# Optimization experiments

Hardware: AMD Instinct MI355X
Metric: run time of the kernel (lower is better)

## Reference

```python
import jax, jax.numpy as jnp
import numpy as np
from jax import lax

ITERATIONS = 8
KT, KH, KW = 3, 7, 7


def _ssm_op(left, right):
    a1, b1 = left
    a2, b2 = right
    return (a1 * a2, a2 * b1 + b2)


def setup_inputs() -> dict:
    key = jax.random.key(0)
    k1, k2, k3 = jax.random.split(key, 3)
    B, T, H, W, C = 1, 16, 64, 64, 128
    x = jax.random.normal(k1, (B, T, H, W, C), dtype=jnp.float32)
    A_kernel = 0.02 * jax.random.normal(k2, (C, KT, KH, KW), dtype=jnp.float32)
    B_kernel = 0.02 * jax.random.normal(k3, (C, KT, KH, KW), dtype=jnp.float32)
    return {"x": x, "A_kernel": A_kernel, "B_kernel": B_kernel}


def _pad_kernel_fft(kern, T, H, W):
    # Place (C, kt, kh, kw) kernel circularly centered into a (C, T, H, W) canvas, FFT it.
    C = kern.shape[0]
    t_idx = (jnp.arange(KT) - KT // 2) % T
    h_idx = (jnp.arange(KH) - KH // 2) % H
    w_idx = (jnp.arange(KW) - KW // 2) % W
    tt, th, tw = jnp.meshgrid(t_idx, h_idx, w_idx, indexing="ij")
    padded = jnp.zeros((C, T, H, W), dtype=kern.dtype).at[:, tt, th, tw].set(kern)
    kf = jnp.fft.fftn(padded, axes=(1, 2, 3))  # (C, T, H, W) complex
    return kf.transpose(1, 2, 3, 0)[None, ...]  # (1, T, H, W, C)


def reference(x, A_kernel, B_kernel):
    B, T, H, W, C = x.shape
    A_stable = 0.9 * jnp.tanh(A_kernel)
    A_f = _pad_kernel_fft(A_stable, T, H, W)   # (1,T,H,W,C)
    B_f = _pad_kernel_fft(B_kernel, T, H, W)   # (1,T,H,W,C)
    x_f = jnp.fft.fftn(x, axes=(1, 2, 3))      # (B,T,H,W,C)
    Bx_f = B_f * x_f
    a_seq = jnp.broadcast_to(A_f, (ITERATIONS, B, T, H, W, C))
    b_seq = jnp.broadcast_to(Bx_f, (ITERATIONS, B, T, H, W, C))
    _, h_all_f = lax.associative_scan(_ssm_op, (a_seq, b_seq), axis=0)
    h_final = jnp.fft.ifftn(h_all_f[-1], axes=(1, 2, 3)).real
    return h_final
```

## Files before the change

### kernel.cpp

```cpp
#include <hip/hip_runtime.h>
#include <hip/hip_fp16.h>
#include <math.h>

#define TT 16
#define HH 64
#define WW 64
#define CC 128

#define LROW(r) (((r) & 0x38) | ((((r) >> 3) ^ (r)) & 7))

__device__ __forceinline__ float2 cadd(float2 a, float2 b){ return make_float2(a.x+b.x, a.y+b.y); }
__device__ __forceinline__ float2 csub(float2 a, float2 b){ return make_float2(a.x-b.x, a.y-b.y); }
__device__ __forceinline__ float2 cmul(float2 a, float2 b) {
    return make_float2(a.x*b.x - a.y*b.y, a.x*b.y + a.y*b.x);
}
__device__ __forceinline__ float2 cmac(float2 acc, float2 a, float2 b) {
    acc.x = fmaf(a.x, b.x, fmaf(-a.y, b.y, acc.x));
    acc.y = fmaf(a.x, b.y, fmaf(a.y, b.x, acc.y));
    return acc;
}
__device__ __forceinline__ float2 csq(float2 a) {
    return make_float2(a.x*a.x - a.y*a.y, 2.f*a.x*a.y);
}

template<int SGN>
__device__ __forceinline__ void dft4(float2 b0, float2 b1, float2 b2, float2 b3,
                                     float2& y0, float2& y1, float2& y2, float2& y3) {
    float2 e0 = cadd(b0, b2), e1 = csub(b0, b2);
    float2 o0 = cadd(b1, b3), o1 = csub(b1, b3);
    y0 = cadd(e0, o0); y2 = csub(e0, o0);
    float2 r = make_float2((float)(-SGN) * o1.y, (float)SGN * o1.x);
    y1 = cadd(e1, r); y3 = csub(e1, r);
}

template<int SGN>
__device__ __forceinline__ void dft8(const float2* a, float2* X) {
    const float C = 0.70710678118654752f;
    float2 E0,E1,E2,E3,O0,O1,O2,O3;
    dft4<SGN>(a[0],a[2],a[4],a[6], E0,E1,E2,E3);
    dft4<SGN>(a[1],a[3],a[5],a[7], O0,O1,O2,O3);
    float2 T1 = make_float2(C*(O1.x - (float)SGN*O1.y), C*((float)SGN*O1.x + O1.y));
    float2 T2 = make_float2((float)(-SGN)*O2.y, (float)SGN*O2.x);
    float2 T3 = make_float2(-C*(O3.x + (float)SGN*O3.y), C*((float)SGN*O3.x - O3.y));
    X[0]=cadd(E0,O0); X[4]=csub(E0,O0);
    X[1]=cadd(E1,T1); X[5]=csub(E1,T1);
    X[2]=cadd(E2,T2); X[6]=csub(E2,T2);
    X[3]=cadd(E3,T3); X[7]=csub(E3,T3);
}

template<int SGN>
__device__ __forceinline__ void dft16(const float2* v, float2* X) {
    const float ct[10] = {1.f, 0.92387953251f, 0.70710678119f, 0.38268343236f, 0.f,
                          0.f, -0.70710678119f, 0.f, 0.f, -0.92387953251f};
    const float st[10] = {0.f, 0.38268343236f, 0.70710678119f, 0.92387953251f, 1.f,
                          0.f, 0.70710678119f, 0.f, 0.f, -0.38268343236f};
    float2 Z[16];
    #pragma unroll
    for (int h0 = 0; h0 < 4; ++h0) {
        float2 y0,y1,y2,y3;
        dft4<SGN>(v[h0], v[4+h0], v[8+h0], v[12+h0], y0,y1,y2,y3);
        float2 ys[4] = {y0,y1,y2,y3};
        #pragma unroll
        for (int k0 = 0; k0 < 4; ++k0) {
            int m = h0 * k0;
            float cc = ct[m], ss = (float)SGN * st[m];
            Z[k0*4 + h0] = make_float2(ys[k0].x*cc - ys[k0].y*ss,
                                       ys[k0].x*ss + ys[k0].y*cc);
        }
    }
    #pragma unroll
    for (int k0 = 0; k0 < 4; ++k0) {
        float2 y0,y1,y2,y3;
        dft4<SGN>(Z[k0*4+0], Z[k0*4+1], Z[k0*4+2], Z[k0*4+3], y0,y1,y2,y3);
        X[k0] = y0; X[k0+4] = y1; X[k0+8] = y2; X[k0+12] = y3;
    }
}

__global__ __launch_bounds__(256) void k_prep(const float* __restrict__ Ak,
                                              const float* __restrict__ Bk,
                                              float2* __restrict__ Ahw,
                                              float2* __restrict__ Bhw) {
    __shared__ float Asl[7][7][64];
    __shared__ float Bsl[7][7][64];
    __shared__ float2 Awl[7][64];
    __shared__ float2 Bwl[7][64];
    __shared__ float2 tw64[64];
    int bid = blockIdx.x;
    int kt = bid / 66;
    int rem = bid % 66;
    int om = rem >> 1, chalf = rem & 1;
    int c0 = chalf * 64;
    int tid = threadIdx.x;
    for (int i = tid; i < 64; i += 256) {
        float s, cq; sincosf(-6.283185307179586f * i / 64.0f, &s, &cq);
        tw64[i] = make_float2(cq, s);
    }
    for (int i = tid; i < 49 * 64; i += 256) {
        int p = i >> 6, cl = i & 63;
        int kh = p / 7, kw = p % 7;
        int idx = (((c0 + cl) * 3 + kt) * 7 + kh) * 7 + kw;
        Asl[kh][kw][cl] = 0.9f * tanhf(Ak[idx]);
        Bsl[kh][kw][cl] = Bk[idx];
    }
    __syncthreads();
    for (int i = tid; i < 7 * 64; i += 256) {
        int kh = i >> 6, cl = i & 63;
        float2 aA = make_float2(0.f,0.f), aB = make_float2(0.f,0.f);
        #pragma unroll
        for (int kw = 0; kw < 7; ++kw) {
            float2 t = tw64[(om * (kw - 3)) & 63];
            float va = Asl[kh][kw][cl], vb = Bsl[kh][kw][cl];
            aA.x = fmaf(va, t.x, aA.x); aA.y = fmaf(va, t.y, aA.y);
            aB.x = fmaf(vb, t.x, aB.x); aB.y = fmaf(vb, t.y, aB.y);
        }
        Awl[kh][cl] = aA; Bwl[kh][cl] = aB;
    }
    __syncthreads();
    for (int i = tid; i < 64 * 64; i += 256) {
        int eta = i >> 6, cl = i & 63;
        float2 aA = make_float2(0.f,0.f), aB = make_float2(0.f,0.f);
        #pragma unroll
        for (int kh = 0; kh < 7; ++kh) {
            float2 t = tw64[(eta * (kh - 3)) & 63];
            aA = cmac(aA, Awl[kh][cl], t);
            aB = cmac(aB, Bwl[kh][cl], t);
        }
        int ep = ((eta & 7) << 3) | (eta >> 3);
        int o = ((kt * 33 + om) * 64 + ep) * 128 + c0 + cl;
        Ahw[o] = aA; Bhw[o] = aB;
    }
}

__global__ __launch_bounds__(256) void p1(const float* __restrict__ x,
                                          __half2* __restrict__ bufh) {
    __shared__ float rf[64][64];
    __shared__ float zim[64][64];
    __shared__ float2 tw64[64];
    int bid = blockIdx.x;
    int chalf = bid & 1, h = (bid >> 1) & 63, t = bid >> 7;
    for (int i = threadIdx.x; i < 64; i += 256) {
        float s, cq; sincosf(-6.283185307179586f * i / 64.0f, &s, &cq);
        tw64[i] = make_float2(cq, s);
    }
    const float4* src4 = (const float4*)(x + (size_t)(t * HH + h) * WW * CC + chalf * 64);
    for (int i = threadIdx.x; i < 1024; i += 256) {
        int w = i >> 4, c4 = i & 15;
        float4 v = src4[w * 32 + c4];
        rf[w][c4*4+0] = v.x; rf[w][c4*4+1] = v.y;
        rf[w][c4*4+2] = v.z; rf[w][c4*4+3] = v.w;
    }
    __syncthreads();
    int c = threadIdx.x & 63, s4 = threadIdx.x >> 6;
    #pragma unroll
    for (int g = 0; g < 2; ++g) {
        int h0 = s4 * 2 + g;
        float2 a[8], Y[8];
        #pragma unroll
        for (int h1 = 0; h1 < 8; ++h1) a[h1] = make_float2(rf[h1 * 8 + h0][c], 0.f);
        dft8<-1>(a, Y);
        #pragma unroll
        for (int k0 = 0; k0 < 8; ++k0) {
            float2 z = cmul(Y[k0], tw64[h0 * k0]);
            rf[k0 * 8 + h0][c] = z.x; zim[k0 * 8 + h0][c] = z.y;
        }
    }
    __syncthreads();
    __half2* dst = bufh + (size_t)(t * HH + h) * WW * CC + chalf * 64 + c;
    #pragma unroll
    for (int g = 0; g < 2; ++g) {
        int k0 = s4 * 2 + g;
        float2 b[8], X[8];
        #pragma unroll
        for (int h0 = 0; h0 < 8; ++h0)
            b[h0] = make_float2(rf[k0 * 8 + h0][c], zim[k0 * 8 + h0][c]);
        dft8<-1>(b, X);
        #pragma unroll
        for (int k1 = 0; k1 < 8; ++k1) {
            int om = k0 + 8 * k1;
            if (om <= 32) dst[(size_t)om * CC] = __float22half2_rn(X[k1]);
        }
    }
}

__global__ __launch_bounds__(256, 4) void pmid(__half2* __restrict__ bufh,
                                               const float2* __restrict__ Ahw,
                                               const float2* __restrict__ Bhw) {
    __shared__ float tre[16][64][4];
    __shared__ float tim[16][64][4];
    int l = (blockIdx.x & 7) * 132 + (blockIdx.x >> 3);
    int om = l >> 5, cc = l & 31;
    int c0 = cc * 4;
    int tid = threadIdx.x;

    int cg = tid & 3, rT = tid >> 2;
    const int PKT = 33 * 64 * 128;
    int kb = (om * 64 + rT) * 128 + c0 + cg;
    float2 A0 = Ahw[kb], A1 = Ahw[kb + PKT], A2 = Ahw[kb + 2*PKT];
    float2 B0 = Bhw[kb], B1 = Bhw[kb + PKT], B2 = Bhw[kb + 2*PKT];

    int d = tid & 7;
    float twc[8], tws[8];
    {
        float s1, c1; sincosf(-6.283185307179586f * d / 64.0f, &s1, &c1);
        twc[0] = 1.f; tws[0] = 0.f;
        #pragma unroll
        for (int k = 1; k < 8; ++k) {
            twc[k] = twc[k-1]*c1 - tws[k-1]*s1;
            tws[k] = twc[k-1]*s1 + tws[k-1]*c1;
        }
    }
    for (int i = tid; i < 2048; i += 256) {
        int t = i >> 7, h = (i >> 1) & 63, p = i & 1;
        size_t e = ((size_t)((t*64 + h)*64 + om))*128 + c0 + 2*p;
        __half2 ha = bufh[e], hb = bufh[e+1];
        float2 v0 = __half22float2(ha), v1 = __half22float2(hb);
        int pr = LROW(h);
        tre[t][pr][2*p]   = v0.x; tim[t][pr][2*p]   = v0.y;
        tre[t][pr][2*p+1] = v1.x; tim[t][pr][2*p+1] = v1.y;
    }
    __syncthreads();
    int cl = (tid >> 3) & 3, ts = tid >> 5;
    #pragma unroll
    for (int q = 0; q < 2; ++q) {
        int t = ts*2 + q;
        float2 a[8], Y[8];
        #pragma unroll
        for (int h1 = 0; h1 < 8; ++h1) {
            int pr = LROW(h1*8 + d);
            a[h1] = make_float2(tre[t][pr][cl], tim[t][pr][cl]);
        }
        dft8<-1>(a, Y);
        #pragma unroll
        for (int k0 = 0; k0 < 8; ++k0) {
            int pr = LROW(k0*8 + d);
            tre[t][pr][cl] = Y[k0].x*twc[k0] - Y[k0].y*tws[k0];
            tim[t][pr][cl] = Y[k0].x*tws[k0] + Y[k0].y*twc[k0];
        }
    }
    __syncthreads();
    #pragma unroll
    for (int q = 0; q < 2; ++q) {
        int t = ts*2 + q;
        float2 a[8], Y[8];
        #pragma unroll
        for (int h0 = 0; h0 < 8; ++h0) {
            int pr = LROW(d*8 + h0);
            a[h0] = make_float2(tre[t][pr][cl], tim[t][pr][cl]);
        }
        dft8<-1>(a, Y);
        #pragma unroll
        for (int k1 = 0; k1 < 8; ++k1) {
            int pr = LROW(d*8 + k1);
            tre[t][pr][cl] = Y[k1].x; tim[t][pr][cl] = Y[k1].y;
        }
    }
    __syncthreads();
    {
        const float CT16[16] = {1.f, 0.9238795325f, 0.7071067812f, 0.3826834324f, 0.f,
                                -0.3826834324f, -0.7071067812f, -0.9238795325f, -1.f,
                                -0.9238795325f, -0.7071067812f, -0.3826834324f, 0.f,
                                0.3826834324f, 0.7071067812f, 0.9238795325f};
        const float ST16[16] = {0.f, 0.3826834324f, 0.7071067812f, 0.9238795325f, 1.f,
                                0.9238795325f, 0.7071067812f, 0.3826834324f, 0.f,
                                -0.3826834324f, -0.7071067812f, -0.9238795325f, -1.f,
                                -0.9238795325f, -0.7071067812f, -0.3826834324f};
        int pr = LROW(rT);
        float2 v[16], X[16];
        #pragma unroll
        for (int t = 0; t < 16; ++t) v[t] = make_float2(tre[t][pr][cg], tim[t][pr][cg]);
        dft16<-1>(v, X);
        #pragma unroll
        for (int ta = 0; ta < 16; ++ta) {
            float2 wv = make_float2(CT16[ta], -ST16[ta]);
            float2 wc = make_float2(CT16[ta],  ST16[ta]);
            float2 Af = A1; Af = cmac(Af, A0, wc); Af = cmac(Af, A2, wv);
            float2 Bf = B1; Bf = cmac(Bf, B0, wc); Bf = cmac(Bf, B2, wv);
            float2 A2q = csq(Af), A4q = csq(A2q);
            float2 S = cmul(make_float2(1.f+Af.x, Af.y), make_float2(1.f+A2q.x, A2q.y));
            S = cmul(S, make_float2(1.f+A4q.x, A4q.y));
            float2 G = cmul(S, Bf);
            X[ta] = cmul(X[ta], G);
        }
        dft16<1>(X, v);
        #pragma unroll
        for (int t = 0; t < 16; ++t) { tre[t][pr][cg] = v[t].x; tim[t][pr][cg] = v[t].y; }
    }
    __syncthreads();
    #pragma unroll
    for (int q = 0; q < 2; ++q) {
        int t = ts*2 + q;
        float2 a[8], Y[8];
        #pragma unroll
        for (int e1 = 0; e1 < 8; ++e1) {
            int pr = LROW(d*8 + e1);
            a[e1] = make_float2(tre[t][pr][cl], tim[t][pr][cl]);
        }
        dft8<1>(a, Y);
        #pragma unroll
        for (int h0 = 0; h0 < 8; ++h0) {
            int pr = LROW(d*8 + h0);
            tre[t][pr][cl] =  Y[h0].x*twc[h0] + Y[h0].y*tws[h0];
            tim[t][pr][cl] = -Y[h0].x*tws[h0] + Y[h0].y*twc[h0];
        }
    }
    __syncthreads();
    #pragma unroll
    for (int q = 0; q < 2; ++q) {
        int t = ts*2 + q;
        float2 a[8], Y[8];
        #pragma unroll
        for (int e0 = 0; e0 < 8; ++e0) {
            int pr = LROW(e0*8 + d);
            a[e0] = make_float2(tre[t][pr][cl], tim[t][pr][cl]);
        }
        dft8<1>(a, Y);
        #pragma unroll
        for (int h1 = 0; h1 < 8; ++h1) {
            int pr = LROW(d + 8*h1);
            tre[t][pr][cl] = Y[h1].x; tim[t][pr][cl] = Y[h1].y;
        }
    }
    __syncthreads();
    for (int i = tid; i < 2048; i += 256) {
        int t = i >> 7, h = (i >> 1) & 63, p = i & 1;
        int pr = LROW(h);
        size_t e = ((size_t)((t*64 + h)*64 + om))*128 + c0 + 2*p;
        bufh[e]   = __float22half2_rn(make_float2(tre[t][pr][2*p]   * 0.015625f,
                                                  tim[t][pr][2*p]   * 0.015625f));
        bufh[e+1] = __float22half2_rn(make_float2(tre[t][pr][2*p+1] * 0.015625f,
                                                  tim[t][pr][2*p+1] * 0.015625f));
    }
}

__global__ __launch_bounds__(256) void p5(const __half2* __restrict__ bufh,
                                          float* __restrict__ out) {
    __shared__ float tre[64][64];
    __shared__ float tim[64][64];
    __shared__ float2 tw64[64];
    int bid = blockIdx.x;
    int chalf = bid & 1, h = (bid >> 1) & 63, t = bid >> 7;
    for (int i = threadIdx.x; i < 64; i += 256) {
        float s, cq; sincosf(6.283185307179586f * i / 64.0f, &s, &cq);
        tw64[i] = make_float2(cq, s);
    }
    const __half2* src = bufh + (size_t)(t * HH + h) * WW * CC + chalf * 64;
    for (int i = threadIdx.x; i < 33 * 64; i += 256) {
        int om = i >> 6, c = i & 63;
        float2 v = __half22float2(src[(size_t)om * CC + c]);
        tre[om][c] = v.x; tim[om][c] = v.y;
        if (om >= 1 && om <= 31) {
            tre[64 - om][c] = v.x; tim[64 - om][c] = -v.y;
        }
    }
    __syncthreads();
    int c = threadIdx.x & 63, s4 = threadIdx.x >> 6;
    #pragma unroll
    for (int g = 0; g < 2; ++g) {
        int h0 = s4 * 2 + g;
        float2 a[8], Y[8];
        #pragma unroll
        for (int h1 = 0; h1 < 8; ++h1)
            a[h1] = make_float2(tre[h1 * 8 + h0][c], tim[h1 * 8 + h0][c]);
        dft8<1>(a, Y);
        #pragma unroll
        for (int k0 = 0; k0 < 8; ++k0) {
            float2 z = cmul(Y[k0], tw64[h0 * k0]);
            tre[k0 * 8 + h0][c] = z.x; tim[k0 * 8 + h0][c] = z.y;
        }
    }
    __syncthreads();
    float* dst = out + (size_t)(t * HH + h) * WW * CC + chalf * 64 + c;
    #pragma unroll
    for (int g = 0; g < 2; ++g) {
        int k0 = s4 * 2 + g;
        float2 b[8], X[8];
        #pragma unroll
        for (int h0 = 0; h0 < 8; ++h0)
            b[h0] = make_float2(tre[k0 * 8 + h0][c], tim[k0 * 8 + h0][c]);
        dft8<1>(b, X);
        #pragma unroll
        for (int k1 = 0; k1 < 8; ++k1)
            dst[(size_t)(k0 + 8 * k1) * CC] = X[k1].x * (1.0f / 1024.0f);
    }
}

extern "C" void kernel_launch(void* const* d_in, const int* in_sizes, int n_in,
                              void* d_out, int out_size, void* d_ws, size_t ws_size,
                              hipStream_t stream) {
    const float* x  = (const float*)d_in[0];
    const float* Ak = (const float*)d_in[1];
    const float* Bk = (const float*)d_in[2];
    float* out = (float*)d_out;

    __half2* bufh = (__half2*)d_ws;
    float2* Ahw = (float2*)(bufh + (size_t)TT * HH * WW * CC);
    float2* Bhw = Ahw + 3 * 33 * 64 * 128;

    hipLaunchKernelGGL(k_prep, dim3(198),  dim3(256), 0, stream, Ak, Bk, Ahw, Bhw);
    hipLaunchKernelGGL(p1,     dim3(2048), dim3(256), 0, stream, x, bufh);
    hipLaunchKernelGGL(pmid,   dim3(1056), dim3(256), 0, stream, bufh, Ahw, Bhw);
    hipLaunchKernelGGL(p5,     dim3(2048), dim3(256), 0, stream, bufh, out);
}
```

Baseline: 70.26 us.

## Store kernel spectra and shared-memory FFT intermediates in half precision, vectorize pmid IO

Kernel spectra A/B written by k_prep become half2 instead of float2, halving their footprint and the bytes pmid reads. p1 and p5 keep their intermediate complex tiles in shared memory as half2 (aliased into one buffer), cutting LDS usage so more blocks can be resident. pmid now loads and stores four half2 values per 16-byte access and raises its launch-bounds occupancy hint from 4 to 5 blocks. The cost is extra fp16 rounding at more stages of the FFT pipeline, which may hurt accuracy, plus an extra barrier in p1 and p5.

Result: no change. 71.57 us (+1.9%).

```diff
diff --git a/kernel.cpp b/kernel.cpp
--- a/kernel.cpp
+++ b/kernel.cpp
@@ -78,8 +78,8 @@
 
 __global__ __launch_bounds__(256) void k_prep(const float* __restrict__ Ak,
                                               const float* __restrict__ Bk,
-                                              float2* __restrict__ Ahw,
-                                              float2* __restrict__ Bhw) {
+                                              __half2* __restrict__ Ahw,
+                                              __half2* __restrict__ Bhw) {
     __shared__ float Asl[7][7][64];
     __shared__ float Bsl[7][7][64];
     __shared__ float2 Awl[7][64];
@@ -127,15 +127,16 @@
         }
         int ep = ((eta & 7) << 3) | (eta >> 3);
         int o = ((kt * 33 + om) * 64 + ep) * 128 + c0 + cl;
-        Ahw[o] = aA; Bhw[o] = aB;
+        Ahw[o] = __float22half2_rn(aA);
+        Bhw[o] = __float22half2_rn(aB);
     }
 }
 
 __global__ __launch_bounds__(256) void p1(const float* __restrict__ x,
                                           __half2* __restrict__ bufh) {
     __shared__ float rf[64][64];
-    __shared__ float zim[64][64];
     __shared__ float2 tw64[64];
+    __half2* zal = (__half2*)&rf[0][0];
     int bid = blockIdx.x;
     int chalf = bid & 1, h = (bid >> 1) & 63, t = bid >> 7;
     for (int i = threadIdx.x; i < 64; i += 256) {
@@ -151,17 +152,25 @@
     }
     __syncthreads();
     int c = threadIdx.x & 63, s4 = threadIdx.x >> 6;
+    float a2[2][8];
+    #pragma unroll
+    for (int g = 0; g < 2; ++g) {
+        int h0 = s4 * 2 + g;
+        #pragma unroll
+        for (int h1 = 0; h1 < 8; ++h1) a2[g][h1] = rf[h1 * 8 + h0][c];
+    }
+    __syncthreads();
     #pragma unroll
     for (int g = 0; g < 2; ++g) {
         int h0 = s4 * 2 + g;
         float2 a[8], Y[8];
         #pragma unroll
-        for (int h1 = 0; h1 < 8; ++h1) a[h1] = make_float2(rf[h1 * 8 + h0][c], 0.f);
+        for (int h1 = 0; h1 < 8; ++h1) a[h1] = make_float2(a2[g][h1], 0.f);
         dft8<-1>(a, Y);
         #pragma unroll
         for (int k0 = 0; k0 < 8; ++k0) {
-            float2 z = cmul(Y[k0], tw64[h0 * k0]);
-            rf[k0 * 8 + h0][c] = z.x; zim[k0 * 8 + h0][c] = z.y;
+            float2 z = cmul(Y[k0], tw64[(h0 * k0) & 63]);
+            zal[(k0 * 8 + h0) * 64 + c] = __float22half2_rn(z);
         }
     }
     __syncthreads();
@@ -172,7 +181,7 @@
         float2 b[8], X[8];
         #pragma unroll
         for (int h0 = 0; h0 < 8; ++h0)
-            b[h0] = make_float2(rf[k0 * 8 + h0][c], zim[k0 * 8 + h0][c]);
+            b[h0] = __half22float2(zal[(k0 * 8 + h0) * 64 + c]);
         dft8<-1>(b, X);
         #pragma unroll
         for (int k1 = 0; k1 < 8; ++k1) {
@@ -182,9 +191,9 @@
     }
 }
 
-__global__ __launch_bounds__(256, 4) void pmid(__half2* __restrict__ bufh,
-                                               const float2* __restrict__ Ahw,
-                                               const float2* __restrict__ Bhw) {
+__global__ __launch_bounds__(256, 5) void pmid(__half2* __restrict__ bufh,
+                                               const __half2* __restrict__ Ahw,
+                                               const __half2* __restrict__ Bhw) {
     __shared__ float tre[16][64][4];
     __shared__ float tim[16][64][4];
     int l = (blockIdx.x & 7) * 132 + (blockIdx.x >> 3);
@@ -195,8 +204,8 @@
     int cg = tid & 3, rT = tid >> 2;
     const int PKT = 33 * 64 * 128;
     int kb = (om * 64 + rT) * 128 + c0 + cg;
-    float2 A0 = Ahw[kb], A1 = Ahw[kb + PKT], A2 = Ahw[kb + 2*PKT];
-    float2 B0 = Bhw[kb], B1 = Bhw[kb + PKT], B2 = Bhw[kb + 2*PKT];
+    __half2 a0h = Ahw[kb], a1h = Ahw[kb + PKT], a2h = Ahw[kb + 2*PKT];
+    __half2 b0h = Bhw[kb], b1h = Bhw[kb + PKT], b2h = Bhw[kb + 2*PKT];
 
     int d = tid & 7;
     float twc[8], tws[8];
@@ -209,14 +218,19 @@
             tws[k] = twc[k-1]*s1 + tws[k-1]*c1;
         }
     }
-    for (int i = tid; i < 2048; i += 256) {
-        int t = i >> 7, h = (i >> 1) & 63, p = i & 1;
-        size_t e = ((size_t)((t*64 + h)*64 + om))*128 + c0 + 2*p;
-        __half2 ha = bufh[e], hb = bufh[e+1];
-        float2 v0 = __half22float2(ha), v1 = __half22float2(hb);
+    for (int i = tid; i < 1024; i += 256) {
+        int t = i >> 6, h = i & 63;
+        const uint4* p4 = (const uint4*)(bufh + (((size_t)(t*64 + h)*64 + om)*128 + c0));
+        uint4 u = *p4;
+        float2 v0 = __half22float2(*(__half2*)&u.x);
+        float2 v1 = __half22float2(*(__half2*)&u.y);
+        float2 v2 = __half22float2(*(__half2*)&u.z);
+        float2 v3 = __half22float2(*(__half2*)&u.w);
         int pr = LROW(h);
-        tre[t][pr][2*p]   = v0.x; tim[t][pr][2*p]   = v0.y;
-        tre[t][pr][2*p+1] = v1.x; tim[t][pr][2*p+1] = v1.y;
+        tre[t][pr][0] = v0.x; tim[t][pr][0] = v0.y;
+        tre[t][pr][1] = v1.x; tim[t][pr][1] = v1.y;
+        tre[t][pr][2] = v2.x; tim[t][pr][2] = v2.y;
+        tre[t][pr][3] = v3.x; tim[t][pr][3] = v3.y;
     }
     __syncthreads();
     int cl = (tid >> 3) & 3, ts = tid >> 5;
@@ -269,6 +283,8 @@
         #pragma unroll
         for (int t = 0; t < 16; ++t) v[t] = make_float2(tre[t][pr][cg], tim[t][pr][cg]);
         dft16<-1>(v, X);
+        float2 A0 = __half22float2(a0h), A1 = __half22float2(a1h), A2 = __half22float2(a2h);
+        float2 B0 = __half22float2(b0h), B1 = __half22float2(b1h), B2 = __half22float2(b2h);
         #pragma unroll
         for (int ta = 0; ta < 16; ++ta) {
             float2 wv = make_float2(CT16[ta], -ST16[ta]);
@@ -321,21 +337,22 @@
         }
     }
     __syncthreads();
-    for (int i = tid; i < 2048; i += 256) {
-        int t = i >> 7, h = (i >> 1) & 63, p = i & 1;
+    const float sc = 0.015625f;
+    for (int i = tid; i < 1024; i += 256) {
+        int t = i >> 6, h = i & 63;
         int pr = LROW(h);
-        size_t e = ((size_t)((t*64 + h)*64 + om))*128 + c0 + 2*p;
-        bufh[e]   = __float22half2_rn(make_float2(tre[t][pr][2*p]   * 0.015625f,
-                                                  tim[t][pr][2*p]   * 0.015625f));
-        bufh[e+1] = __float22half2_rn(make_float2(tre[t][pr][2*p+1] * 0.015625f,
-                                                  tim[t][pr][2*p+1] * 0.015625f));
+        uint4 u;
+        *(__half2*)&u.x = __float22half2_rn(make_float2(tre[t][pr][0]*sc, tim[t][pr][0]*sc));
+        *(__half2*)&u.y = __float22half2_rn(make_float2(tre[t][pr][1]*sc, tim[t][pr][1]*sc));
+        *(__half2*)&u.z = __float22half2_rn(make_float2(tre[t][pr][2]*sc, tim[t][pr][2]*sc));
+        *(__half2*)&u.w = __float22half2_rn(make_float2(tre[t][pr][3]*sc, tim[t][pr][3]*sc));
+        *(uint4*)(bufh + (((size_t)(t*64 + h)*64 + om)*128 + c0)) = u;
     }
 }
 
 __global__ __launch_bounds__(256) void p5(const __half2* __restrict__ bufh,
                                           float* __restrict__ out) {
-    __shared__ float tre[64][64];
-    __shared__ float tim[64][64];
+    __shared__ __half2 zal[64][64];
     __shared__ float2 tw64[64];
     int bid = blockIdx.x;
     int chalf = bid & 1, h = (bid >> 1) & 63, t = bid >> 7;
@@ -346,26 +363,32 @@
     const __half2* src = bufh + (size_t)(t * HH + h) * WW * CC + chalf * 64;
     for (int i = threadIdx.x; i < 33 * 64; i += 256) {
         int om = i >> 6, c = i & 63;
-        float2 v = __half22float2(src[(size_t)om * CC + c]);
-        tre[om][c] = v.x; tim[om][c] = v.y;
+        __half2 v = src[(size_t)om * CC + c];
+        zal[om][c] = v;
         if (om >= 1 && om <= 31) {
-            tre[64 - om][c] = v.x; tim[64 - om][c] = -v.y;
+            __half2 m = v; m.y = __hneg(v.y);
+            zal[64 - om][c] = m;
         }
     }
     __syncthreads();
     int c = threadIdx.x & 63, s4 = threadIdx.x >> 6;
+    float2 a2[2][8];
     #pragma unroll
     for (int g = 0; g < 2; ++g) {
         int h0 = s4 * 2 + g;
-        float2 a[8], Y[8];
-        #pragma unroll
-        for (int h1 = 0; h1 < 8; ++h1)
-            a[h1] = make_float2(tre[h1 * 8 + h0][c], tim[h1 * 8 + h0][c]);
-        dft8<1>(a, Y);
+        #pragma unroll
+        for (int h1 = 0; h1 < 8; ++h1) a2[g][h1] = __half22float2(zal[h1 * 8 + h0][c]);
+    }
+    __syncthreads();
+    #pragma unroll
+    for (int g = 0; g < 2; ++g) {
+        int h0 = s4 * 2 + g;
+        float2 Y[8];
+        dft8<1>(a2[g], Y);
         #pragma unroll
         for (int k0 = 0; k0 < 8; ++k0) {
-            float2 z = cmul(Y[k0], tw64[h0 * k0]);
-            tre[k0 * 8 + h0][c] = z.x; tim[k0 * 8 + h0][c] = z.y;
+            float2 z = cmul(Y[k0], tw64[(h0 * k0) & 63]);
+            zal[k0 * 8 + h0][c] = __float22half2_rn(z);
         }
     }
     __syncthreads();
@@ -376,7 +399,7 @@
         float2 b[8], X[8];
         #pragma unroll
         for (int h0 = 0; h0 < 8; ++h0)
-            b[h0] = make_float2(tre[k0 * 8 + h0][c], tim[k0 * 8 + h0][c]);
+            b[h0] = __half22float2(zal[k0 * 8 + h0][c]);
         dft8<1>(b, X);
         #pragma unroll
         for (int k1 = 0; k1 < 8; ++k1)
@@ -393,8 +416,8 @@
     float* out = (float*)d_out;
 
     __half2* bufh = (__half2*)d_ws;
-    float2* Ahw = (float2*)(bufh + (size_t)TT * HH * WW * CC);
-    float2* Bhw = Ahw + 3 * 33 * 64 * 128;
+    __half2* Ahw = bufh + (size_t)TT * HH * WW * CC;
+    __half2* Bhw = Ahw + 3 * 33 * 64 * 128;
 
     hipLaunchKernelGGL(k_prep, dim3(198),  dim3(256), 0, stream, Ak, Bk, Ahw, Bhw);
     hipLaunchKernelGGL(p1,     dim3(2048), dim3(256), 0, stream, x, bufh);
```
